# Optimization experiments

Measured on AMD Instinct MI355X. Metric: run time of the kernel, lower is better.

Reference implementation:

```python
import jax, jax.numpy as jnp
import numpy as np

K = 2
BN_EPS = 1e-5


def setup_inputs() -> dict:
    key = jax.random.key(0)
    k1, k2, k3 = jax.random.split(key, 3)
    B, C, H, W, D, O = 4, 128, 32, 32, 32, 128
    x = jax.random.normal(k1, (B, C, H, W, D), dtype=jnp.float32)
    conv_w = jax.random.normal(k2, (O, 2 * C), dtype=jnp.float32) * 0.02  # 1x1x1 conv kernel
    conv_b = jax.random.normal(k3, (O,), dtype=jnp.float32) * 0.02
    bn_gamma = jnp.ones((O,), dtype=jnp.float32)
    bn_beta = jnp.zeros((O,), dtype=jnp.float32)
    return {"x": x, "conv_w": conv_w, "conv_b": conv_b,
            "bn_gamma": bn_gamma, "bn_beta": bn_beta}


def _axis_running_max(x, x_j, axis, dim):
    # torch.cat([x[..., -i:], x[..., :-i]], axis) == jnp.roll(x, i, axis)
    shifts = jnp.arange(K, dim, K)

    def step(carry, s):
        diff = x - jnp.roll(x, s, axis=axis)
        return jnp.maximum(carry, diff), None

    x_j, _ = jax.lax.scan(step, x_j, shifts)
    return x_j


def reference(x, conv_w, conv_b, bn_gamma, bn_beta):
    B, C, H, W, D = x.shape
    x_j = jnp.zeros_like(x)
    x_j = _axis_running_max(x, x_j, 2, H)
    x_j = _axis_running_max(x, x_j, 3, W)
    x_j = _axis_running_max(x, x_j, 4, D)
    x_j = jax.lax.stop_gradient(x_j)  # original detaches every x_j update

    xc = jnp.concatenate([x, x_j], axis=1)  # [B, 2C, H, W, D]
    # 1x1x1 Conv3d == per-voxel channel GEMM
    y = jnp.einsum('bchwd,oc->bohwd', xc, conv_w) + conv_b[None, :, None, None, None]

    # BatchNorm3d, training mode (batch statistics over B,H,W,D)
    mean = y.mean(axis=(0, 2, 3, 4), keepdims=True)
    var = ((y - mean) ** 2).mean(axis=(0, 2, 3, 4), keepdims=True)
    yn = (y - mean) * jax.lax.rsqrt(var + BN_EPS)
    yn = yn * bn_gamma[None, :, None, None, None] + bn_beta[None, :, None, None, None]

    # torch nn.GELU default is exact erf form
    return jax.nn.gelu(yn, approximate=False)
```

## Files before the change

kernel.cpp:

```cpp
#include <hip/hip_runtime.h>
#include <hip/hip_bf16.h>

#define BB 4
#define CCH 128
#define C2 256
#define OO 128
#define NVOX 32768
#define NTOT (BB*NVOX)

typedef __attribute__((ext_vector_type(4))) float f32x4;
typedef __attribute__((ext_vector_type(8))) short s16x8;
typedef __attribute__((ext_vector_type(4))) unsigned int u32x4;
typedef unsigned int u32;
typedef unsigned short u16;

#define SWZ(r) ((((r)>>3) ^ (r)) & 7)

__device__ __forceinline__ float bf2f(short s){
  union { u32 i; float f; } cv; cv.i = ((u32)(u16)s) << 16; return cv.f;
}
__device__ __forceinline__ short f2bf(float f){
  union { __hip_bfloat16 h; short s; } cv; cv.h = __float2bfloat16(f); return cv.s;
}
__device__ __forceinline__ u32 pack2(float a, float b){
  return ((u32)(u16)f2bf(a)) | (((u32)(u16)f2bf(b)) << 16);
}
__device__ __forceinline__ float ulo(u32 r){
  union { u32 i; float f; } cv; cv.i = r << 16; return cv.f;
}
__device__ __forceinline__ float uhi(u32 r){
  union { u32 i; float f; } cv; cv.i = r & 0xffff0000u; return cv.f;
}
__device__ __forceinline__ float bfr(float f){ return bf2f(f2bf(f)); }

__global__ __launch_bounds__(256) void k_convw(const float* __restrict__ w, short* __restrict__ wb){
  int i = blockIdx.x*256 + threadIdx.x;
  wb[i] = f2bf(w[i]);
}

__global__ __launch_bounds__(1024) void k_tab(const float* __restrict__ x,
                                              u32* __restrict__ tw, u32* __restrict__ th,
                                              short* __restrict__ xbf){
  int t = threadIdx.x;
  u32 bc = blockIdx.x;
  const float* __restrict__ src = x + (size_t)bc*NVOX;
  int a = t >> 5, d = t & 31;
  {
    float m1[2] = {1e30f,1e30f}, m2[2] = {1e30f,1e30f};
    #pragma unroll
    for(int w=0;w<32;w++){
      float v = bfr(src[a*1024 + w*32 + d]);
      int p = w & 1;
      m2[p] = fminf(m2[p], fmaxf(m1[p], v));
      m1[p] = fminf(m1[p], v);
    }
    u32* r = tw + (size_t)bc*2048 + a*64;
    r[d]      = pack2(m1[0], m2[0]);
    r[32 + d] = pack2(m1[1], m2[1]);
  }
  {
    float m1[2] = {1e30f,1e30f}, m2[2] = {1e30f,1e30f};
    #pragma unroll
    for(int h=0;h<32;h++){
      float v = bfr(src[h*1024 + a*32 + d]);
      int p = h & 1;
      m2[p] = fminf(m2[p], fmaxf(m1[p], v));
      m1[p] = fminf(m1[p], v);
    }
    u32* r = th + (size_t)bc*2048 + a*32;
    r[d]        = pack2(m1[0], m2[0]);
    r[1024 + d] = pack2(m1[1], m2[1]);
  }
  {
    const float* pl = src + t*32;
    u32 xp[16];
    #pragma unroll
    for(int g=0;g<8;g++){
      f32x4 v = *(const f32x4*)(pl + g*4);
      xp[g*2]   = pack2(v[0], v[1]);
      xp[g*2+1] = pack2(v[2], v[3]);
    }
    short* dst = xbf + (size_t)bc*NVOX + t*32;
    #pragma unroll
    for(int g=0;g<4;g++)
      *(u32x4*)(dst + g*8) = (u32x4){xp[g*4],xp[g*4+1],xp[g*4+2],xp[g*4+3]};
  }
}

__global__ __launch_bounds__(256) void k_gemm(const short* __restrict__ xbf, const short* __restrict__ wb,
                                              const u32* __restrict__ tw, const u32* __restrict__ th,
                                              short* __restrict__ y, float* __restrict__ part){
  __shared__ __align__(16) char lds[65536];
  char* ldsJ = lds + 32768;
  u32 orig = blockIdx.x;
  u32 xcd = orig & 7, slot = orig >> 3;
  u32 b    = xcd >> 1;
  u32 vblk = (xcd & 1)*128 + slot;
  u32 blk  = b*256 + vblk;
  u32 vbase = vblk * 128;
  int t = threadIdx.x;
  int wave = t >> 6, lane = t & 63;
  int wr = wave >> 1, wc = wave & 1;
  int l15 = lane & 15, l4 = lane >> 4;

  {
    int v0   = (t & 15) * 8;
    int line = (t & 15) >> 2;
    int d0   = (t & 3) * 8;
    int cb2  = 2 * (t >> 4);
    int h  = vbase >> 10;
    int w  = ((vbase >> 5) & 31) + line;
    #pragma unroll
    for(int q=0;q<4;q++){
      int c = cb2 + 32*q;
      const short* pe = xbf + ((size_t)(b*CCH + c))*NVOX + vbase + v0;
      s16x8 ra = *(const s16x8*)(pe);
      s16x8 rb = *(const s16x8*)(pe + NVOX);
      u32 pr[8];
      #pragma unroll
      for(int e=0;e<8;e++)
        pr[e] = ((u32)(u16)ra[e]) | (((u32)(u16)rb[e]) << 16);
      #pragma unroll
      for(int e=0;e<8;e++){
        int v = v0 + e;
        *(u32*)(lds + v*256 + ((((c>>3) ^ SWZ(v))<<4) | ((c&7)<<1))) = pr[e];
      }
      float m1e[2]={1e30f,1e30f}, m2e[2]={1e30f,1e30f};
      float m1o[2]={1e30f,1e30f}, m2o[2]={1e30f,1e30f};
      #pragma unroll
      for(int e=0;e<8;e++){
        int p = e & 1;
        float xe = ulo(pr[e]), xo = uhi(pr[e]);
        m2e[p] = fminf(m2e[p], fmaxf(m1e[p], xe)); m1e[p] = fminf(m1e[p], xe);
        m2o[p] = fminf(m2o[p], fmaxf(m1o[p], xo)); m1o[p] = fminf(m1o[p], xo);
      }
      #pragma unroll
      for(int mk=1;mk<=2;mk<<=1){
        #pragma unroll
        for(int p=0;p<2;p++){
          float b1, b2;
          b1 = __shfl_xor(m1e[p], mk); b2 = __shfl_xor(m2e[p], mk);
          m2e[p] = fminf(fmaxf(m1e[p], b1), fminf(m2e[p], b2));
          m1e[p] = fminf(m1e[p], b1);
          b1 = __shfl_xor(m1o[p], mk); b2 = __shfl_xor(m2o[p], mk);
          m2o[p] = fminf(fmaxf(m1o[p], b1), fminf(m2o[p], b2));
          m1o[p] = fminf(m1o[p], b1);
        }
      }
      size_t bce = ((size_t)b*CCH + c)*2048;
      const u32* twE = tw + bce + h*64 + (w&1)*32 + d0;
      const u32* thE = th + bce + (h&1)*1024 + w*32 + d0;
      u32x4 we0 = *(const u32x4*)(twE),        we1 = *(const u32x4*)(twE + 4);
      u32x4 wo0 = *(const u32x4*)(twE + 2048), wo1 = *(const u32x4*)(twE + 2052);
      u32x4 he0 = *(const u32x4*)(thE),        he1 = *(const u32x4*)(thE + 4);
      u32x4 ho0 = *(const u32x4*)(thE + 2048), ho1 = *(const u32x4*)(thE + 2052);
      #pragma unroll
      for(int e=0;e<8;e++){
        int p = e & 1;
        float xe = ulo(pr[e]), xo = uhi(pr[e]);
        u32 we = (e<4) ? we0[e] : we1[e-4];
        u32 wo = (e<4) ? wo0[e] : wo1[e-4];
        u32 he = (e<4) ? he0[e] : he1[e-4];
        u32 ho = (e<4) ? ho0[e] : ho1[e-4];
        float mDe = (xe == m1e[p]) ? m2e[p] : m1e[p];
        float mDo = (xo == m1o[p]) ? m2o[p] : m1o[p];
        float w1e = ulo(we); float mWe = (xe == w1e) ? uhi(we) : w1e;
        float w1o = ulo(wo); float mWo = (xo == w1o) ? uhi(wo) : w1o;
        float h1e = ulo(he); float mHe = (xe == h1e) ? uhi(he) : h1e;
        float h1o = ulo(ho); float mHo = (xo == h1o) ? uhi(ho) : h1o;
        float je = fmaxf(0.f, xe - fminf(mDe, fminf(mWe, mHe)));
        float jo = fmaxf(0.f, xo - fminf(mDo, fminf(mWo, mHo)));
        int v = v0 + e;
        *(u32*)(ldsJ + v*256 + ((((c>>3) ^ SWZ(v))<<4) | ((c&7)<<1))) = pack2(je, jo);
      }
    }
  }
  __syncthreads();

  f32x4 acc[4][4];
  #pragma unroll
  for(int mt=0;mt<4;mt++)
    #pragma unroll
    for(int nt=0;nt<4;nt++) acc[mt][nt] = (f32x4){0.f,0.f,0.f,0.f};
  #pragma unroll
  for(int kc=0;kc<2;kc++){
    const char* tile = (kc == 0) ? lds : ldsJ;
    #pragma unroll
    for(int ks=0;ks<4;ks++){
      int kk = ks*32 + l4*8;
      s16x8 afrag[4], bfrag[4];
      #pragma unroll
      for(int nt=0;nt<4;nt++){
        int vloc = wc*64 + nt*16 + l15;
        bfrag[nt] = *(const s16x8*)(tile + vloc*256 + (((kk>>3) ^ SWZ(vloc))<<4));
      }
      #pragma unroll
      for(int mt=0;mt<4;mt++){
        int o = wr*64 + mt*16 + l15;
        afrag[mt] = *(const s16x8*)(wb + o*C2 + kc*128 + kk);
      }
      #pragma unroll
      for(int mt=0;mt<4;mt++)
        #pragma unroll
        for(int nt=0;nt<4;nt++)
          acc[mt][nt] = __builtin_amdgcn_mfma_f32_16x16x32_bf16(afrag[mt], bfrag[nt], acc[mt][nt], 0,0,0);
    }
  }

  __syncthreads();
  #pragma unroll
  for(int mt=0;mt<4;mt++){
    #pragma unroll
    for(int nt=0;nt<4;nt++){
      int vcol = wc*64 + nt*16 + l15;
      #pragma unroll
      for(int r=0;r<4;r++){
        int o = wr*64 + mt*16 + l4*4 + r;
        *(short*)(lds + o*256 + ((((vcol>>3) ^ SWZ(o))<<4) | ((vcol&7)<<1))) = f2bf(acc[mt][nt][r]);
      }
    }
  }
  __syncthreads();
  short* __restrict__ yb = y + (size_t)b*OO*NVOX + vbase;
  #pragma unroll
  for(int q=0;q<8;q++){
    int p = t + q*256;
    int o = p >> 4, vs = (p & 15) * 8;
    s16x8 val = *(const s16x8*)(lds + o*256 + ((((vs>>3) ^ SWZ(o))<<4)));
    *(s16x8*)(yb + (size_t)o*NVOX + vs) = val;
  }

  {
    int o = t >> 1, vh = t & 1;
    float sm = 0.f, ss = 0.f;
    #pragma unroll
    for(int k=0;k<8;k++){
      int vs = vh*64 + k*8;
      s16x8 val = *(const s16x8*)(lds + o*256 + ((((vs>>3) ^ SWZ(o))<<4)));
      #pragma unroll
      for(int e=0;e<8;e++){ float f = bf2f(val[e]); sm += f; ss += f*f; }
    }
    sm += __shfl_xor(sm, 1);
    ss += __shfl_xor(ss, 1);
    if(vh == 0){
      float* pp = part + ((size_t)blk*OO + o)*2;
      pp[0] = sm; pp[1] = ss;
    }
  }
}

__global__ __launch_bounds__(256) void k_statsf(const float* __restrict__ part, float* __restrict__ stats){
  int o = blockIdx.x, t = threadIdx.x;
  float sm = 0.f, ss = 0.f;
  #pragma unroll
  for(int k=0;k<4;k++){
    int blk = t + k*256;
    const float* pp = part + ((size_t)blk*OO + o)*2;
    sm += pp[0]; ss += pp[1];
  }
  __shared__ float rs[256], rss[256];
  rs[t] = sm; rss[t] = ss;
  __syncthreads();
  for(int k=128;k>0;k>>=1){
    if(t<k){ rs[t]+=rs[t+k]; rss[t]+=rss[t+k]; }
    __syncthreads();
  }
  if(t==0){
    float inv = 1.0f/(float)NTOT;
    float mean = rs[0]*inv;
    float var = rss[0]*inv - mean*mean;
    stats[2*o]   = mean;
    stats[2*o+1] = rsqrtf(var + 1e-5f);
  }
}

__global__ __launch_bounds__(256) void k_bngelu(const short* __restrict__ y, const float* __restrict__ stats,
                                                const float* __restrict__ gamma, const float* __restrict__ beta,
                                                float* __restrict__ out){
  size_t base = ((size_t)blockIdx.x*256 + threadIdx.x)*8;
  int o = (int)((base >> 15) & 127);
  float mean = stats[2*o], rstd = stats[2*o+1];
  float g  = gamma[o]*rstd;
  float be = beta[o] - mean*g;
  s16x8 u = *(const s16x8*)(y + base);
  f32x4 r0, r1;
  #pragma unroll
  for(int e=0;e<8;e++){
    float yn = bf2f(u[e])*g + be;
    float ge = 0.5f*yn*(1.0f + erff(yn*0.70710678118654752f));
    if(e<4) r0[e] = ge; else r1[e-4] = ge;
  }
  *(f32x4*)(out + base)     = r0;
  *(f32x4*)(out + base + 4) = r1;
}

extern "C" void kernel_launch(void* const* d_in, const int* in_sizes, int n_in,
                              void* d_out, int out_size, void* d_ws, size_t ws_size,
                              hipStream_t stream) {
  (void)in_sizes; (void)n_in; (void)out_size; (void)ws_size;
  const float* x     = (const float*)d_in[0];
  const float* cw    = (const float*)d_in[1];
  const float* gamma = (const float*)d_in[3];
  const float* beta  = (const float*)d_in[4];
  float* out = (float*)d_out;

  char* ws = (char*)d_ws;
  short* wb    = (short*)ws;
  short* y     = (short*)(ws + 65536);
  float* stats = (float*)(ws + 65536 + (size_t)BB*OO*NVOX*2);
  float* part  = stats + 256;
  u32* tw  = (u32*)d_out;
  u32* th  = tw + (size_t)512*2048;
  short* xbf = (short*)(th + (size_t)512*2048);

  k_convw <<<dim3((OO*C2)/256),     dim3(256), 0, stream>>>(cw, wb);
  k_tab   <<<dim3(BB*CCH),         dim3(1024), 0, stream>>>(x, tw, th, xbf);
  k_gemm  <<<dim3(BB*(NVOX/128)),  dim3(256), 0, stream>>>(xbf, wb, tw, th, y, part);
  k_statsf<<<dim3(OO),             dim3(256), 0, stream>>>(part, stats);
  k_bngelu<<<dim3((NTOT*OO)/2048), dim3(256), 0, stream>>>(y, stats, gamma, beta, out);
}
```

Measured before the change: 98.79 us.

## Vectorize table kernel with fused bf16 copy; double GEMM block to 512 threads

The table kernel now reads x as float4 with lanes split along the reduction axis, merges partial min-pairs through shuffles, and writes the bf16 copy of x during the W-axis pass. This removes the separate third pass over x and the scalar strided loads. The GEMM kernel moves to 512 threads with 8 waves (2x4), so each wave computes half as many N tiles and each thread stages half as many channels. The aim is more parallelism and latency hiding per block, at the cost of more shuffle work and a higher per-block thread count.

```diff
diff --git a/kernel.cpp b/kernel.cpp
--- a/kernel.cpp
+++ b/kernel.cpp
@@ -11,6 +11,7 @@
 typedef __attribute__((ext_vector_type(4))) float f32x4;
 typedef __attribute__((ext_vector_type(8))) short s16x8;
 typedef __attribute__((ext_vector_type(4))) unsigned int u32x4;
+typedef __attribute__((ext_vector_type(2))) unsigned int u32x2;
 typedef unsigned int u32;
 typedef unsigned short u16;
 
@@ -32,6 +33,11 @@
   union { u32 i; float f; } cv; cv.i = r & 0xffff0000u; return cv.f;
 }
 __device__ __forceinline__ float bfr(float f){ return bf2f(f2bf(f)); }
+
+#define MERGE2(m1v, m2v, b1v, b2v) { \
+  float _b1 = (b1v), _b2 = (b2v); \
+  m2v = fminf(fmaxf(m1v, _b1), fminf(m2v, _b2)); \
+  m1v = fminf(m1v, _b1); }
 
 __global__ __launch_bounds__(256) void k_convw(const float* __restrict__ w, short* __restrict__ wb){
   int i = blockIdx.x*256 + threadIdx.x;
@@ -44,50 +50,79 @@
   int t = threadIdx.x;
   u32 bc = blockIdx.x;
   const float* __restrict__ src = x + (size_t)bc*NVOX;
-  int a = t >> 5, d = t & 31;
   {
-    float m1[2] = {1e30f,1e30f}, m2[2] = {1e30f,1e30f};
-    #pragma unroll
-    for(int w=0;w<32;w++){
-      float v = bfr(src[a*1024 + w*32 + d]);
-      int p = w & 1;
-      m2[p] = fminf(m2[p], fmaxf(m1[p], v));
-      m1[p] = fminf(m1[p], v);
-    }
-    u32* r = tw + (size_t)bc*2048 + a*64;
-    r[d]      = pack2(m1[0], m2[0]);
-    r[32 + d] = pack2(m1[1], m2[1]);
+    int h = t >> 5, dq = (t >> 2) & 7, wq = t & 3;
+    int d0 = dq*4;
+    float m1[2][4], m2[2][4];
+    #pragma unroll
+    for(int p=0;p<2;p++)
+      #pragma unroll
+      for(int j=0;j<4;j++){ m1[p][j]=1e30f; m2[p][j]=1e30f; }
+    short* xd = xbf + (size_t)bc*NVOX + h*1024 + d0;
+    #pragma unroll
+    for(int i=0;i<8;i++){
+      int w = wq*8 + i;
+      f32x4 v = *(const f32x4*)(src + h*1024 + w*32 + d0);
+      float r0=bfr(v[0]), r1=bfr(v[1]), r2=bfr(v[2]), r3=bfr(v[3]);
+      *(u32x2*)(xd + w*32) = (u32x2){pack2(r0,r1), pack2(r2,r3)};
+      int p = i & 1;
+      m2[p][0]=fminf(m2[p][0],fmaxf(m1[p][0],r0)); m1[p][0]=fminf(m1[p][0],r0);
+      m2[p][1]=fminf(m2[p][1],fmaxf(m1[p][1],r1)); m1[p][1]=fminf(m1[p][1],r1);
+      m2[p][2]=fminf(m2[p][2],fmaxf(m1[p][2],r2)); m1[p][2]=fminf(m1[p][2],r2);
+      m2[p][3]=fminf(m2[p][3],fmaxf(m1[p][3],r3)); m1[p][3]=fminf(m1[p][3],r3);
+    }
+    #pragma unroll
+    for(int mk=1;mk<=2;mk<<=1)
+      #pragma unroll
+      for(int p=0;p<2;p++)
+        #pragma unroll
+        for(int j=0;j<4;j++)
+          MERGE2(m1[p][j], m2[p][j], __shfl_xor(m1[p][j], mk), __shfl_xor(m2[p][j], mk));
+    if(wq == 0){
+      u32* r = tw + (size_t)bc*2048 + h*64 + d0;
+      *(u32x4*)(r)      = (u32x4){pack2(m1[0][0],m2[0][0]), pack2(m1[0][1],m2[0][1]),
+                                  pack2(m1[0][2],m2[0][2]), pack2(m1[0][3],m2[0][3])};
+      *(u32x4*)(r + 32) = (u32x4){pack2(m1[1][0],m2[1][0]), pack2(m1[1][1],m2[1][1]),
+                                  pack2(m1[1][2],m2[1][2]), pack2(m1[1][3],m2[1][3])};
+    }
   }
   {
-    float m1[2] = {1e30f,1e30f}, m2[2] = {1e30f,1e30f};
-    #pragma unroll
-    for(int h=0;h<32;h++){
-      float v = bfr(src[h*1024 + a*32 + d]);
-      int p = h & 1;
-      m2[p] = fminf(m2[p], fmaxf(m1[p], v));
-      m1[p] = fminf(m1[p], v);
-    }
-    u32* r = th + (size_t)bc*2048 + a*32;
-    r[d]        = pack2(m1[0], m2[0]);
-    r[1024 + d] = pack2(m1[1], m2[1]);
-  }
-  {
-    const float* pl = src + t*32;
-    u32 xp[16];
-    #pragma unroll
-    for(int g=0;g<8;g++){
-      f32x4 v = *(const f32x4*)(pl + g*4);
-      xp[g*2]   = pack2(v[0], v[1]);
-      xp[g*2+1] = pack2(v[2], v[3]);
-    }
-    short* dst = xbf + (size_t)bc*NVOX + t*32;
-    #pragma unroll
-    for(int g=0;g<4;g++)
-      *(u32x4*)(dst + g*8) = (u32x4){xp[g*4],xp[g*4+1],xp[g*4+2],xp[g*4+3]};
-  }
-}
-
-__global__ __launch_bounds__(256) void k_gemm(const short* __restrict__ xbf, const short* __restrict__ wb,
+    int w = t >> 5, dq = (t >> 2) & 7, hq = t & 3;
+    int d0 = dq*4;
+    float m1[2][4], m2[2][4];
+    #pragma unroll
+    for(int p=0;p<2;p++)
+      #pragma unroll
+      for(int j=0;j<4;j++){ m1[p][j]=1e30f; m2[p][j]=1e30f; }
+    #pragma unroll
+    for(int i=0;i<8;i++){
+      int h = hq*8 + i;
+      f32x4 v = *(const f32x4*)(src + h*1024 + w*32 + d0);
+      float r0=bfr(v[0]), r1=bfr(v[1]), r2=bfr(v[2]), r3=bfr(v[3]);
+      int p = i & 1;
+      m2[p][0]=fminf(m2[p][0],fmaxf(m1[p][0],r0)); m1[p][0]=fminf(m1[p][0],r0);
+      m2[p][1]=fminf(m2[p][1],fmaxf(m1[p][1],r1)); m1[p][1]=fminf(m1[p][1],r1);
+      m2[p][2]=fminf(m2[p][2],fmaxf(m1[p][2],r2)); m1[p][2]=fminf(m1[p][2],r2);
+      m2[p][3]=fminf(m2[p][3],fmaxf(m1[p][3],r3)); m1[p][3]=fminf(m1[p][3],r3);
+    }
+    #pragma unroll
+    for(int mk=1;mk<=2;mk<<=1)
+      #pragma unroll
+      for(int p=0;p<2;p++)
+        #pragma unroll
+        for(int j=0;j<4;j++)
+          MERGE2(m1[p][j], m2[p][j], __shfl_xor(m1[p][j], mk), __shfl_xor(m2[p][j], mk));
+    if(hq == 0){
+      u32* r = th + (size_t)bc*2048 + w*32 + d0;
+      *(u32x4*)(r)        = (u32x4){pack2(m1[0][0],m2[0][0]), pack2(m1[0][1],m2[0][1]),
+                                    pack2(m1[0][2],m2[0][2]), pack2(m1[0][3],m2[0][3])};
+      *(u32x4*)(r + 1024) = (u32x4){pack2(m1[1][0],m2[1][0]), pack2(m1[1][1],m2[1][1]),
+                                    pack2(m1[1][2],m2[1][2]), pack2(m1[1][3],m2[1][3])};
+    }
+  }
+}
+
+__global__ __launch_bounds__(512, 2) void k_gemm(const short* __restrict__ xbf, const short* __restrict__ wb,
                                               const u32* __restrict__ tw, const u32* __restrict__ th,
                                               short* __restrict__ y, float* __restrict__ part){
   __shared__ __align__(16) char lds[65536];
@@ -100,7 +135,7 @@
   u32 vbase = vblk * 128;
   int t = threadIdx.x;
   int wave = t >> 6, lane = t & 63;
-  int wr = wave >> 1, wc = wave & 1;
+  int wr = wave >> 2, wc = wave & 3;
   int l15 = lane & 15, l4 = lane >> 4;
 
   {
@@ -111,8 +146,8 @@
     int h  = vbase >> 10;
     int w  = ((vbase >> 5) & 31) + line;
     #pragma unroll
-    for(int q=0;q<4;q++){
-      int c = cb2 + 32*q;
+    for(int q=0;q<2;q++){
+      int c = cb2 + 64*q;
       const short* pe = xbf + ((size_t)(b*CCH + c))*NVOX + vbase + v0;
       s16x8 ra = *(const s16x8*)(pe);
       s16x8 rb = *(const s16x8*)(pe + NVOX);
@@ -138,13 +173,8 @@
       for(int mk=1;mk<=2;mk<<=1){
         #pragma unroll
         for(int p=0;p<2;p++){
-          float b1, b2;
-          b1 = __shfl_xor(m1e[p], mk); b2 = __shfl_xor(m2e[p], mk);
-          m2e[p] = fminf(fmaxf(m1e[p], b1), fminf(m2e[p], b2));
-          m1e[p] = fminf(m1e[p], b1);
-          b1 = __shfl_xor(m1o[p], mk); b2 = __shfl_xor(m2o[p], mk);
-          m2o[p] = fminf(fmaxf(m1o[p], b1), fminf(m2o[p], b2));
-          m1o[p] = fminf(m1o[p], b1);
+          MERGE2(m1e[p], m2e[p], __shfl_xor(m1e[p], mk), __shfl_xor(m2e[p], mk));
+          MERGE2(m1o[p], m2o[p], __shfl_xor(m1o[p], mk), __shfl_xor(m2o[p], mk));
         }
       }
       size_t bce = ((size_t)b*CCH + c)*2048;
@@ -177,21 +207,21 @@
   }
   __syncthreads();
 
-  f32x4 acc[4][4];
+  f32x4 acc[4][2];
   #pragma unroll
   for(int mt=0;mt<4;mt++)
     #pragma unroll
-    for(int nt=0;nt<4;nt++) acc[mt][nt] = (f32x4){0.f,0.f,0.f,0.f};
+    for(int nt=0;nt<2;nt++) acc[mt][nt] = (f32x4){0.f,0.f,0.f,0.f};
   #pragma unroll
   for(int kc=0;kc<2;kc++){
     const char* tile = (kc == 0) ? lds : ldsJ;
     #pragma unroll
     for(int ks=0;ks<4;ks++){
       int kk = ks*32 + l4*8;
-      s16x8 afrag[4], bfrag[4];
-      #pragma unroll
-      for(int nt=0;nt<4;nt++){
-        int vloc = wc*64 + nt*16 + l15;
+      s16x8 afrag[4], bfrag[2];
+      #pragma unroll
+      for(int nt=0;nt<2;nt++){
+        int vloc = wc*32 + nt*16 + l15;
         bfrag[nt] = *(const s16x8*)(tile + vloc*256 + (((kk>>3) ^ SWZ(vloc))<<4));
       }
       #pragma unroll
@@ -202,7 +232,7 @@
       #pragma unroll
       for(int mt=0;mt<4;mt++)
         #pragma unroll
-        for(int nt=0;nt<4;nt++)
+        for(int nt=0;nt<2;nt++)
           acc[mt][nt] = __builtin_amdgcn_mfma_f32_16x16x32_bf16(afrag[mt], bfrag[nt], acc[mt][nt], 0,0,0);
     }
   }
@@ -211,8 +241,8 @@
   #pragma unroll
   for(int mt=0;mt<4;mt++){
     #pragma unroll
-    for(int nt=0;nt<4;nt++){
-      int vcol = wc*64 + nt*16 + l15;
+    for(int nt=0;nt<2;nt++){
+      int vcol = wc*32 + nt*16 + l15;
       #pragma unroll
       for(int r=0;r<4;r++){
         int o = wr*64 + mt*16 + l4*4 + r;
@@ -223,25 +253,25 @@
   __syncthreads();
   short* __restrict__ yb = y + (size_t)b*OO*NVOX + vbase;
   #pragma unroll
-  for(int q=0;q<8;q++){
-    int p = t + q*256;
+  for(int q=0;q<4;q++){
+    int p = t + q*512;
     int o = p >> 4, vs = (p & 15) * 8;
     s16x8 val = *(const s16x8*)(lds + o*256 + ((((vs>>3) ^ SWZ(o))<<4)));
     *(s16x8*)(yb + (size_t)o*NVOX + vs) = val;
   }
 
   {
-    int o = t >> 1, vh = t & 1;
+    int o = t >> 2, vh = t & 3;
     float sm = 0.f, ss = 0.f;
     #pragma unroll
-    for(int k=0;k<8;k++){
-      int vs = vh*64 + k*8;
+    for(int k=0;k<4;k++){
+      int vs = vh*32 + k*8;
       s16x8 val = *(const s16x8*)(lds + o*256 + ((((vs>>3) ^ SWZ(o))<<4)));
       #pragma unroll
       for(int e=0;e<8;e++){ float f = bf2f(val[e]); sm += f; ss += f*f; }
     }
-    sm += __shfl_xor(sm, 1);
-    ss += __shfl_xor(ss, 1);
+    sm += __shfl_xor(sm, 1); ss += __shfl_xor(ss, 1);
+    sm += __shfl_xor(sm, 2); ss += __shfl_xor(ss, 2);
     if(vh == 0){
       float* pp = part + ((size_t)blk*OO + o)*2;
       pp[0] = sm; pp[1] = ss;
@@ -315,7 +345,7 @@
 
   k_convw <<<dim3((OO*C2)/256),     dim3(256), 0, stream>>>(cw, wb);
   k_tab   <<<dim3(BB*CCH),         dim3(1024), 0, stream>>>(x, tw, th, xbf);
-  k_gemm  <<<dim3(BB*(NVOX/128)),  dim3(256), 0, stream>>>(xbf, wb, tw, th, y, part);
+  k_gemm  <<<dim3(BB*(NVOX/128)),  dim3(512), 0, stream>>>(xbf, wb, tw, th, y, part);
   k_statsf<<<dim3(OO),             dim3(256), 0, stream>>>(part, stats);
   k_bngelu<<<dim3((NTOT*OO)/2048), dim3(256), 0, stream>>>(y, stats, gamma, beta, out);
 }
```

Result: slower. 104.9 us (+6.2%).
